# Kernel optimization log

Measured on AMD Instinct MI355X. Metric: run time of the kernel, lower is better.

The kernel has to match this reference:

```python
import jax, jax.numpy as jnp
from jax import lax
import numpy as np

# ---- constants (from Coords2Elec init kwargs) ----
BOX = 128          # box_size
RES = 1.0          # resolution (Angstrom / voxel)
EPS_IN = 6.5
EPS_OUT = 79.0
ION = 1.0          # ion_size
WAT = 1.4          # wat_size (water probe radius)
ASIGMA = 2.0
KAPPA02 = 0.8486   # debye_length kwarg, passed to solver as kappa0^2
QCONV = 7046.52    # charge_conv
D = 2              # gaussian sharpness divisor
W = 9              # scatter support window per axis (covers ~2.7 sigma)
N_ITER = 20        # Jacobi sweeps for the Poisson-Boltzmann solve

# staggered-grid offsets for the 4 eps channels: face-centered x/y/z + ion grid
OFFSETS = ((0.5, 0.0, 0.0), (0.0, 0.5, 0.0), (0.0, 0.0, 0.5), (0.5, 0.5, 0.5))


def _scatter_gauss(coords, sigma, mask, offset):
    """Scatter per-atom Gaussian density onto a staggered [B,BOX,BOX,BOX] grid.
    coords [B,N,3], sigma [B,N], mask [B,N], offset: 3 floats in voxel units."""
    B, N, _ = coords.shape
    off = jnp.asarray(offset, coords.dtype)
    offs = jnp.arange(W)
    # window base index so that grid node positions (idx+off)*RES bracket the atom
    base = jnp.floor(coords / RES - off).astype(jnp.int32) - W // 2     # [B,N,3]
    idx = base[..., None] + offs                                         # [B,N,3,W]
    gpos = (idx.astype(coords.dtype) + off[None, None, :, None]) * RES   # [B,N,3,W]
    d2 = (gpos - coords[..., None]) ** 2
    wax = jnp.exp(-d2 / (2.0 * sigma[:, :, None, None] ** 2))            # [B,N,3,W]
    w = (wax[:, :, 0, :, None, None] * wax[:, :, 1, None, :, None]
         * wax[:, :, 2, None, None, :]) * mask[:, :, None, None, None]   # [B,N,W,W,W]
    b_idx = jnp.broadcast_to(jnp.arange(B)[:, None, None, None, None], w.shape)
    ix = jnp.broadcast_to(idx[:, :, 0, :, None, None], w.shape)
    iy = jnp.broadcast_to(idx[:, :, 1, None, :, None], w.shape)
    iz = jnp.broadcast_to(idx[:, :, 2, None, None, :], w.shape)
    grid = jnp.zeros((B, BOX, BOX, BOX), coords.dtype)
    return grid.at[b_idx, ix, iy, iz].add(w, mode='drop')


def _scatter_q(coords, charge, mask):
    """Trilinear scatter of per-atom charges onto node grid [B,BOX,BOX,BOX]."""
    B, N, _ = coords.shape
    u = coords / RES
    i0 = jnp.floor(u).astype(jnp.int32)                 # [B,N,3]
    f = u - i0
    wpair = jnp.stack([1.0 - f, f], -1)                 # [B,N,3,2]
    ipair = jnp.stack([i0, i0 + 1], -1)                 # [B,N,3,2]
    w = (wpair[:, :, 0, :, None, None] * wpair[:, :, 1, None, :, None]
         * wpair[:, :, 2, None, None, :]) * (charge * mask)[:, :, None, None, None]
    b_idx = jnp.broadcast_to(jnp.arange(B)[:, None, None, None, None], w.shape)
    ix = jnp.broadcast_to(ipair[:, :, 0, :, None, None], w.shape)
    iy = jnp.broadcast_to(ipair[:, :, 1, None, :, None], w.shape)
    iz = jnp.broadcast_to(ipair[:, :, 2, None, None, :], w.shape)
    grid = jnp.zeros((B, BOX, BOX, BOX), coords.dtype)
    return grid.at[b_idx, ix, iy, iz].add(w, mode='drop')


def _face_nb(a, axis):
    """Face eps of the (i-1) cell along axis; boundary padded with EPS_OUT."""
    lead = jnp.full_like(lax.slice_in_dim(a, 0, 1, axis=axis), EPS_OUT)
    return jnp.concatenate([lead, lax.slice_in_dim(a, 0, a.shape[axis] - 1, axis=axis)], axis=axis)


def _phi_nb(phi, axis, d):
    """Neighbor potential phi[i+d] along spatial axis, zero (Dirichlet) outside."""
    z = jnp.zeros_like(lax.slice_in_dim(phi, 0, 1, axis=axis))
    if d > 0:
        return jnp.concatenate([lax.slice_in_dim(phi, 1, phi.shape[axis], axis=axis), z], axis=axis)
    return jnp.concatenate([z, lax.slice_in_dim(phi, 0, phi.shape[axis] - 1, axis=axis)], axis=axis)


def _qeps2phi(Q, Eps):
    """Fixed-iteration Jacobi solve of the linearized Poisson-Boltzmann stencil."""
    ex, ey, ez, ek = Eps[:, 0], Eps[:, 1], Eps[:, 2], Eps[:, 3]
    exm, eym, ezm = _face_nb(ex, 1), _face_nb(ey, 2), _face_nb(ez, 3)
    lam = jnp.clip((ek - EPS_IN) / (EPS_OUT - EPS_IN), 0.0, 1.0)  # ion accessibility
    denom = ex + exm + ey + eym + ez + ezm + KAPPA02 * RES * RES * lam
    src = 4.0 * jnp.pi * Q * RES

    def body(i, phi):
        num = (ex * _phi_nb(phi, 1, +1) + exm * _phi_nb(phi, 1, -1)
               + ey * _phi_nb(phi, 2, +1) + eym * _phi_nb(phi, 2, -1)
               + ez * _phi_nb(phi, 3, +1) + ezm * _phi_nb(phi, 3, -1) + src)
        return num / denom

    return lax.fori_loop(0, N_ITER, body, jnp.zeros_like(Q))


def setup_inputs() -> dict:
    key = jax.random.key(0)
    k1, k2, k3, k4 = jax.random.split(key, 4)
    B, N = 4, 4096
    coords = jax.random.uniform(k1, (B, N, 3), jnp.float32) * ((BOX - 1) * RES)
    charges = jax.random.normal(k2, (B, N), jnp.float32) * 0.5     # partial charges
    radii = 1.0 + jax.random.uniform(k3, (B, N), jnp.float32)      # 1..2 Angstrom
    assigned_params = jnp.stack([charges, radii], -1)              # [B,N,2]
    num_atoms = jax.random.randint(k4, (B,), N // 2, N + 1, jnp.int32)
    return {"coords": coords, "assigned_params": assigned_params, "num_atoms": num_atoms}


def reference(coords, assigned_params, num_atoms):
    B, N, _ = coords.shape
    mask = (jnp.arange(N)[None, :] < num_atoms[:, None]).astype(coords.dtype)
    charge = assigned_params[..., 0]
    radii = assigned_params[..., 1]
    sig_eps = (radii + WAT) / D   # solvent-excluded Gaussian width
    sig_ion = (radii + ION) / D   # ion-excluded Gaussian width
    rho = jnp.stack([
        _scatter_gauss(coords, sig_eps if c < 3 else sig_ion, mask, OFFSETS[c])
        for c in range(4)], axis=1)                     # [B,4,BOX,BOX,BOX]
    rho = jnp.clip(rho, 0.0, 1.0)
    eps = rho * (EPS_IN - EPS_OUT) + EPS_OUT
    q = _scatter_q(coords, charge, mask) * QCONV        # [B,BOX,BOX,BOX]
    phi = _qeps2phi(q, eps)
    return q, eps, phi
```

## Files before the change

kernel.cpp:

```cpp
#include <hip/hip_runtime.h>
#include <hip/hip_fp16.h>
#include <math.h>

static constexpr int   B_    = 4;
static constexpr int   N_    = 4096;
static constexpr int   BOX_  = 128;
static constexpr long long VOX_ = 1LL * BOX_ * BOX_ * BOX_;
static constexpr float EPS_IN_C  = 6.5f;
static constexpr float EPS_OUT_C = 79.0f;
static constexpr float QCONV_C   = 7046.52f;
static constexpr float KAPPA02_C = 0.8486f;
static constexpr float FOURPI_C  = 12.566370614359172f;

__global__ void scatter_q_kernel(const float* __restrict__ coords,
                                 const float* __restrict__ params,
                                 const int*   __restrict__ num_atoms,
                                 float* __restrict__ q)
{
    int a = blockIdx.x * blockDim.x + threadIdx.x;
    if (a >= B_ * N_) return;
    int b = a >> 12;
    int n = a & (N_ - 1);
    if (n >= num_atoms[b]) return;

    float cx = coords[3 * a + 0];
    float cy = coords[3 * a + 1];
    float cz = coords[3 * a + 2];
    float chg = params[2 * a + 0] * QCONV_C;

    int ix0 = (int)floorf(cx), iy0 = (int)floorf(cy), iz0 = (int)floorf(cz);
    float fx = cx - (float)ix0, fy = cy - (float)iy0, fz = cz - (float)iz0;
    float wx[2] = {1.0f - fx, fx};
    float wy[2] = {1.0f - fy, fy};
    float wz[2] = {1.0f - fz, fz};

    float* qb = q + (long long)b * VOX_;
#pragma unroll
    for (int dx = 0; dx < 2; ++dx) {
        int ix = ix0 + dx;
        if ((unsigned)ix >= 128u) continue;
#pragma unroll
        for (int dy = 0; dy < 2; ++dy) {
            int iy = iy0 + dy;
            if ((unsigned)iy >= 128u) continue;
#pragma unroll
            for (int dz = 0; dz < 2; ++dz) {
                int iz = iz0 + dz;
                if ((unsigned)iz >= 128u) continue;
                atomicAdd(&qb[((long long)ix * 128 + iy) * 128 + iz],
                          chg * wx[dx] * wy[dy] * wz[dz]);
            }
        }
    }
}

#define CAND_CAP 512
#define CHUNK 32

__global__ void eps_gather_v2(const float* __restrict__ coords,
                              const float* __restrict__ params,
                              const int*   __restrict__ num_atoms,
                              float* __restrict__ eps)
{
    int tileId = blockIdx.x;
    int b  = tileId >> 12;
    int t  = tileId & 4095;
    int tx = ((t >> 8) & 15) << 3;
    int ty = ((t >> 4) & 15) << 3;
    int tz = (t & 15) << 3;

    __shared__ float sx[CAND_CAP], sy[CAND_CAP], sz[CAND_CAP], sr[CAND_CAP];
    __shared__ float wts[CHUNK][9][8];
    __shared__ int s_cnt;
    if (threadIdx.x == 0) s_cnt = 0;
    __syncthreads();

    int na = num_atoms[b];
    const float* cb = coords + (size_t)b * N_ * 3;
    const float* pb = params + (size_t)b * N_ * 2;

    float lox = (float)tx - 4.0f, hix = (float)tx + 12.5f;
    float loy = (float)ty - 4.0f, hiy = (float)ty + 12.5f;
    float loz = (float)tz - 4.0f, hiz = (float)tz + 12.5f;
    bool wx_ = (tx == 120), wy_ = (ty == 120), wz_ = (tz == 120);
    for (int n = threadIdx.x; n < na; n += blockDim.x) {
        float cx = cb[3 * n], cy = cb[3 * n + 1], cz = cb[3 * n + 2];
        bool okx = (cx >= lox && cx < hix) || (wx_ && cx < 4.5f);
        bool oky = (cy >= loy && cy < hiy) || (wy_ && cy < 4.5f);
        bool okz = (cz >= loz && cz < hiz) || (wz_ && cz < 4.5f);
        if (okx && oky && okz) {
            int slot = atomicAdd(&s_cnt, 1);
            if (slot < CAND_CAP) {
                sx[slot] = cx; sy[slot] = cy; sz[slot] = cz;
                sr[slot] = pb[2 * n + 1];
            }
        }
    }
    __syncthreads();
    int cnt = min(s_cnt, CAND_CAP);

    int lz = threadIdx.x & 7;
    int ly = (threadIdx.x >> 3) & 7;
    int lx = threadIdx.x >> 6;

    float r0 = 0.0f, r1 = 0.0f, r2 = 0.0f, r3 = 0.0f;

    for (int k0 = 0; k0 < cnt; k0 += CHUNK) {
        int nC = min(CHUNK, cnt - k0);
        __syncthreads();
        for (int w = threadIdx.x; w < nC * 72; w += 512) {
            int ka  = w / 72;
            int rem = w - ka * 72;
            int vi  = rem >> 3;
            int pos = rem & 7;
            int axis = vi / 3, var = vi - axis * 3;
            int k = k0 + ka;
            float c     = (axis == 0) ? sx[k] : (axis == 1) ? sy[k] : sz[k];
            int   torig = (axis == 0) ? tx    : (axis == 1) ? ty    : tz;
            float r = sr[k];
            float sig = (var == 2) ? (r + 1.0f) * 0.5f : (r + 1.4f) * 0.5f;
            float off = (var == 0) ? 0.0f : 0.5f;
            float inv2s2 = 1.0f / (2.0f * sig * sig);
            int i = torig + pos;
            int base = (int)floorf(c - off) - 4;
            float wv = 0.0f;
            if ((unsigned)(i - base) <= 8u) {
                float d = (float)i + off - c;
                wv = expf(-d * d * inv2s2);
            } else if ((unsigned)(i - 128 - base) <= 8u) {
                float d = (float)(i - 128) + off - c;
                wv = expf(-d * d * inv2s2);
            }
            wts[ka][vi][pos] = wv;
        }
        __syncthreads();
        for (int ka = 0; ka < nC; ++ka) {
            float xE0 = wts[ka][0][lx], xE5 = wts[ka][1][lx], xI5 = wts[ka][2][lx];
            float yE0 = wts[ka][3][ly], yE5 = wts[ka][4][ly], yI5 = wts[ka][5][ly];
            float zE0 = wts[ka][6][lz], zE5 = wts[ka][7][lz], zI5 = wts[ka][8][lz];
            r0 += xE5 * yE0 * zE0;
            r1 += xE0 * yE5 * zE0;
            r2 += xE0 * yE0 * zE5;
            r3 += xI5 * yI5 * zI5;
        }
    }

    int ix = tx + lx, iy = ty + ly, iz = tz + lz;
    size_t sp = ((size_t)ix * 128 + iy) * 128 + iz;
    float* eb = eps + (size_t)b * 4 * VOX_;
    eb[sp]                    = EPS_OUT_C + (EPS_IN_C - EPS_OUT_C) * fminf(fmaxf(r0, 0.0f), 1.0f);
    eb[sp + (size_t)VOX_]     = EPS_OUT_C + (EPS_IN_C - EPS_OUT_C) * fminf(fmaxf(r1, 0.0f), 1.0f);
    eb[sp + (size_t)VOX_ * 2] = EPS_OUT_C + (EPS_IN_C - EPS_OUT_C) * fminf(fmaxf(r2, 0.0f), 1.0f);
    eb[sp + (size_t)VOX_ * 3] = EPS_OUT_C + (EPS_IN_C - EPS_OUT_C) * fminf(fmaxf(r3, 0.0f), 1.0f);
}

__global__ void coef_pack4(const float* __restrict__ eps,
                           const float* __restrict__ q,
                           uint4* __restrict__ coef,
                           float* __restrict__ phi1)
{
    int tid = blockIdx.x * blockDim.x + threadIdx.x;
    size_t g4 = (size_t)tid * 4;
    int b  = (int)(g4 >> 21);
    size_t sp = g4 & (size_t)(VOX_ - 1);
    int x  = (int)(sp >> 14);
    int y  = (int)((sp >> 7) & 127);
    int z4 = (int)(sp & 127);

    const float* E = eps + (size_t)b * 4 * (size_t)VOX_;
    float4 ex4 = *reinterpret_cast<const float4*>(E + sp);
    float4 ey4 = *reinterpret_cast<const float4*>(E + sp + (size_t)VOX_);
    float4 ez4 = *reinterpret_cast<const float4*>(E + sp + (size_t)VOX_ * 2);
    float4 ek4 = *reinterpret_cast<const float4*>(E + sp + (size_t)VOX_ * 3);
    float4 eo  = make_float4(EPS_OUT_C, EPS_OUT_C, EPS_OUT_C, EPS_OUT_C);
    float4 exm4 = (x > 0) ? *reinterpret_cast<const float4*>(E + sp - 16384) : eo;
    float4 eym4 = (y > 0) ? *reinterpret_cast<const float4*>(E + sp + (size_t)VOX_ - 128) : eo;
    float ezm0  = (z4 > 0) ? E[sp + (size_t)VOX_ * 2 - 1] : EPS_OUT_C;
    float4 q4  = *reinterpret_cast<const float4*>(q + g4);

    float exA[4]  = {ex4.x, ex4.y, ex4.z, ex4.w};
    float eyA[4]  = {ey4.x, ey4.y, ey4.z, ey4.w};
    float ezA[4]  = {ez4.x, ez4.y, ez4.z, ez4.w};
    float ekA[4]  = {ek4.x, ek4.y, ek4.z, ek4.w};
    float exmA[4] = {exm4.x, exm4.y, exm4.z, exm4.w};
    float eymA[4] = {eym4.x, eym4.y, eym4.z, eym4.w};
    float ezmA[4] = {ezm0, ez4.x, ez4.y, ez4.z};
    float qA[4]   = {q4.x, q4.y, q4.z, q4.w};

    float ph[4];
#pragma unroll
    for (int j = 0; j < 4; ++j) {
        float lam = (ekA[j] - EPS_IN_C) / (EPS_OUT_C - EPS_IN_C);
        lam = fminf(fmaxf(lam, 0.0f), 1.0f);
        float denom = exA[j] + exmA[j] + eyA[j] + eymA[j] + ezA[j] + ezmA[j]
                    + KAPPA02_C * lam;
        float rcp = 1.0f / denom;

        __half2 h01 = __floats2half2_rn(exA[j] * rcp, exmA[j] * rcp);
        __half2 h23 = __floats2half2_rn(eyA[j] * rcp, eymA[j] * rcp);
        __half2 h45 = __floats2half2_rn(ezA[j] * rcp, ezmA[j] * rcp);
        __half2 h67 = __floats2half2_rn(FOURPI_C * qA[j] * rcp, 0.0f);
        uint4 u;
        u.x = *(unsigned int*)&h01;
        u.y = *(unsigned int*)&h23;
        u.z = *(unsigned int*)&h45;
        u.w = *(unsigned int*)&h67;
        coef[g4 + j] = u;
        ph[j] = __half22float2(h67).x;
    }
    *reinterpret_cast<float4*>(phi1 + g4) = make_float4(ph[0], ph[1], ph[2], ph[3]);
}

#define TY 8
#define TZ 32
#define RY (TY + 2)
#define RZ (TZ + 2)
#define PYD (TY + 4)
#define PZD (TZ + 4)
#define SEG 16

__global__ __launch_bounds__(256)
void jacobi_f2p(const uint4* __restrict__ coef,
                const float* __restrict__ pin,
                float* __restrict__ pout)
{
    int bid = blockIdx.x;
    int xs = bid & 7;
    int zt = (bid >> 3) & 3;
    int yt = (bid >> 5) & 15;
    int b  = bid >> 9;
    int x_lo = xs * SEG, x_hi = x_lo + SEG - 1;
    int y0 = yt * TY, z0 = zt * TZ;

    __shared__ float P[3][PYD * PZD];
    __shared__ float S[3][RY * RZ];

    int tid = threadIdx.x;
    int oy = tid >> 5, oz = tid & 31;

    const uint4* cb = coef + (size_t)b * VOX_;
    const float* pb = pin  + (size_t)b * VOX_;
    float*       ob = pout + (size_t)b * VOX_;

    int e1_i  = (oy + 1) * RZ + (oz + 1);
    int g1y = y0 + oy, g1z = z0 + oz;
    int e1_off = g1y * 128 + g1z;
    int e1_p0 = (oy + 2) * PZD + (oz + 2);
    bool has2 = (tid < 84);
    int e2_ry = 0, e2_rz = 0;
    if (tid < 34)      { e2_ry = 0;      e2_rz = tid; }
    else if (tid < 68) { e2_ry = RY - 1; e2_rz = tid - 34; }
    else if (tid < 84) { int t2 = tid - 68; e2_ry = 1 + (t2 >> 1); e2_rz = (t2 & 1) * (RZ - 1); }
    int e2_i = e2_ry * RZ + e2_rz;
    int g2y = y0 - 1 + e2_ry, g2z = z0 - 1 + e2_rz;
    bool e2_ok = ((unsigned)g2y < 128u) && ((unsigned)g2z < 128u);
    int e2_off = min(max(g2y, 0), 127) * 128 + min(max(g2z, 0), 127);
    int e2_p0 = (e2_ry + 1) * PZD + (e2_rz + 1);
    int p1_py = tid / PZD, p1_pz = tid - p1_py * PZD;
    int p1y = y0 - 2 + p1_py, p1z = z0 - 2 + p1_pz;
    bool p1_ok = ((unsigned)p1y < 128u) && ((unsigned)p1z < 128u);
    int p1_off = min(max(p1y, 0), 127) * 128 + min(max(p1z, 0), 127);
    int p2i = tid + 256;
    bool hasP2 = (p2i < PYD * PZD);
    int p2_py = p2i / PZD, p2_pz = p2i - p2_py * PZD;
    int p2y = y0 - 2 + p2_py, p2z = z0 - 2 + p2_pz;
    bool p2_ok = hasP2 && ((unsigned)p2y < 128u) && ((unsigned)p2z < 128u);
    int p2_off = min(max(p2y, 0), 127) * 128 + min(max(p2z, 0), 127);

    const float* ps0 = pb + (size_t)min(max(x_lo - 2, 0), 127) * 16384;
    float pfA = ps0[p1_off];
    float pfB = hasP2 ? ps0[p2_off] : 0.0f;
    uint4 cf1 = make_uint4(0u, 0u, 0u, 0u);
    uint4 cf2 = make_uint4(0u, 0u, 0u, 0u);
    uint4 hold = make_uint4(0u, 0u, 0u, 0u);
    uint4 cnew = make_uint4(0u, 0u, 0u, 0u);

    for (int x = x_lo - 2; x <= x_hi + 2; ++x) {
        int s0 = (x + 3) % 3;
        int s1 = (x + 2) % 3;
        int s2 = (x + 1) % 3;
        bool xin = (x >= 0 && x < 128);

        P[s0][tid] = (xin && p1_ok) ? pfA : 0.0f;
        if (hasP2) P[s0][p2i] = (xin && p2_ok) ? pfB : 0.0f;
        asm volatile("s_waitcnt lgkmcnt(0)" ::: "memory");
        __builtin_amdgcn_s_barrier();

        if (x < x_hi + 2) {
            const float* ps = pb + (size_t)min(max(x + 1, 0), 127) * 16384;
            pfA = ps[p1_off];
            if (hasP2) pfB = ps[p2_off];
        }

        if (x >= x_lo) {
            int k = x - 1;
            bool kin = ((unsigned)k < 128u);
            {
                float v = 0.0f;
                if (kin) {
                    const __half2* h = reinterpret_cast<const __half2*>(&cf1);
                    float2 a01 = __half22float2(h[0]);
                    float2 a23 = __half22float2(h[1]);
                    float2 a45 = __half22float2(h[2]);
                    float2 a67 = __half22float2(h[3]);
                    v = a01.x * P[s0][e1_p0]
                      + a01.y * P[s2][e1_p0]
                      + a23.x * P[s1][e1_p0 + PZD]
                      + a23.y * P[s1][e1_p0 - PZD]
                      + a45.x * P[s1][e1_p0 + 1]
                      + a45.y * P[s1][e1_p0 - 1]
                      + a67.x;
                }
                S[s1][e1_i] = v;
                cnew = cf1;
            }
            if (has2) {
                float v = 0.0f;
                if (kin && e2_ok) {
                    const __half2* h = reinterpret_cast<const __half2*>(&cf2);
                    float2 a01 = __half22float2(h[0]);
                    float2 a23 = __half22float2(h[1]);
                    float2 a45 = __half22float2(h[2]);
                    float2 a67 = __half22float2(h[3]);
                    v = a01.x * P[s0][e2_p0]
                      + a01.y * P[s2][e2_p0]
                      + a23.x * P[s1][e2_p0 + PZD]
                      + a23.y * P[s1][e2_p0 - PZD]
                      + a45.x * P[s1][e2_p0 + 1]
                      + a45.y * P[s1][e2_p0 - 1]
                      + a67.x;
                }
                S[s1][e2_i] = v;
            }
        }
        if (x >= x_lo - 1 && x <= x_hi + 1) {
            const uint4* cs = cb + (size_t)min(max(x, 0), 127) * 16384;
            cf1 = cs[e1_off];
            if (has2) cf2 = cs[e2_off];
        }
        asm volatile("s_waitcnt lgkmcnt(0)" ::: "memory");
        __builtin_amdgcn_s_barrier();

        int xo = x - 2;
        if (xo >= x_lo) {
            const __half2* h = reinterpret_cast<const __half2*>(&hold);
            float2 a01 = __half22float2(h[0]);
            float2 a23 = __half22float2(h[1]);
            float2 a45 = __half22float2(h[2]);
            float2 a67 = __half22float2(h[3]);
            int j0 = e1_i;
            float out = a01.x * S[s1][j0]
                      + a01.y * S[s0][j0]
                      + a23.x * S[s2][j0 + RZ]
                      + a23.y * S[s2][j0 - RZ]
                      + a45.x * S[s2][j0 + 1]
                      + a45.y * S[s2][j0 - 1]
                      + a67.x;
            ob[(size_t)xo * 16384 + e1_off] = out;
        }
        hold = cnew;
    }
}

__global__ void jacobi_v3(const uint4* __restrict__ coef,
                          const float* __restrict__ pin,
                          float* __restrict__ pout)
{
    int tid = blockIdx.x * blockDim.x + threadIdx.x;
    size_t g4 = (size_t)tid * 4;
    int z4 = (int)(g4 & 127);
    int y  = (int)((g4 >> 7) & 127);
    int x  = (int)((g4 >> 14) & 127);

    float4 pcv = *reinterpret_cast<const float4*>(pin + g4);
    float4 z4v = make_float4(0.f, 0.f, 0.f, 0.f);
    float4 pxpv = (x < 127) ? *reinterpret_cast<const float4*>(pin + g4 + 16384) : z4v;
    float4 pxmv = (x > 0)   ? *reinterpret_cast<const float4*>(pin + g4 - 16384) : z4v;
    float4 pypv = (y < 127) ? *reinterpret_cast<const float4*>(pin + g4 + 128)   : z4v;
    float4 pymv = (y > 0)   ? *reinterpret_cast<const float4*>(pin + g4 - 128)   : z4v;
    float zpE = (z4 < 124) ? pin[g4 + 4] : 0.0f;
    float zmE = (z4 > 0)   ? pin[g4 - 1] : 0.0f;

    float pxp[4] = {pxpv.x, pxpv.y, pxpv.z, pxpv.w};
    float pxm[4] = {pxmv.x, pxmv.y, pxmv.z, pxmv.w};
    float pyp[4] = {pypv.x, pypv.y, pypv.z, pypv.w};
    float pym[4] = {pymv.x, pymv.y, pymv.z, pymv.w};
    float pzp[4] = {pcv.y, pcv.z, pcv.w, zpE};
    float pzm[4] = {zmE, pcv.x, pcv.y, pcv.z};

    float out[4];
#pragma unroll
    for (int j = 0; j < 4; ++j) {
        uint4 cu = coef[g4 + j];
        const __half2* h = reinterpret_cast<const __half2*>(&cu);
        float2 a01 = __half22float2(h[0]);
        float2 a23 = __half22float2(h[1]);
        float2 a45 = __half22float2(h[2]);
        float2 a67 = __half22float2(h[3]);
        out[j] = a01.x * pxp[j] + a01.y * pxm[j]
               + a23.x * pyp[j] + a23.y * pym[j]
               + a45.x * pzp[j] + a45.y * pzm[j]
               + a67.x;
    }
    *reinterpret_cast<float4*>(pout + g4) = make_float4(out[0], out[1], out[2], out[3]);
}

__global__ void jacobi_v2(const float* __restrict__ eps,
                          const float* __restrict__ q,
                          const float* __restrict__ pin,
                          float* __restrict__ pout)
{
    int bxy = blockIdx.x;
    int b = bxy >> 14;
    int x = (bxy >> 7) & 127;
    int y = bxy & 127;
    int z = threadIdx.x;

    size_t sp = ((size_t)x * 128 + y) * 128 + z;
    size_t g  = (size_t)b * (size_t)VOX_ + sp;
    const float* E = eps + (size_t)b * 4 * (size_t)VOX_;

    float ex = E[sp];
    float ey = E[sp + (size_t)VOX_];
    float ez = E[sp + (size_t)VOX_ * 2];
    float ek = E[sp + (size_t)VOX_ * 3];
    float exm = (x > 0) ? E[sp - 16384]                 : EPS_OUT_C;
    float eym = (y > 0) ? E[sp + (size_t)VOX_ - 128]    : EPS_OUT_C;
    float ezm = (z > 0) ? E[sp + (size_t)VOX_ * 2 - 1]  : EPS_OUT_C;

    float lam = (ek - EPS_IN_C) / (EPS_OUT_C - EPS_IN_C);
    lam = fminf(fmaxf(lam, 0.0f), 1.0f);
    float denom = ex + exm + ey + eym + ez + ezm + KAPPA02_C * lam;

    float pxp = (x < 127) ? pin[g + 16384] : 0.0f;
    float pxm = (x > 0)   ? pin[g - 16384] : 0.0f;
    float pyp = (y < 127) ? pin[g + 128]   : 0.0f;
    float pym = (y > 0)   ? pin[g - 128]   : 0.0f;
    float pzp = (z < 127) ? pin[g + 1]     : 0.0f;
    float pzm = (z > 0)   ? pin[g - 1]     : 0.0f;

    float num = ex * pxp + exm * pxm + ey * pyp + eym * pym
              + ez * pzp + ezm * pzm + FOURPI_C * q[g];
    pout[g] = num / denom;
}

extern "C" void kernel_launch(void* const* d_in, const int* in_sizes, int n_in,
                              void* d_out, int out_size, void* d_ws, size_t ws_size,
                              hipStream_t stream)
{
    const float* coords    = (const float*)d_in[0];
    const float* params    = (const float*)d_in[1];
    const int*   num_atoms = (const int*)d_in[2];

    float* q   = (float*)d_out;
    float* eps = q + (size_t)B_ * VOX_;
    float* phi = eps + (size_t)B_ * 4 * VOX_;

    hipMemsetAsync(q, 0, (size_t)B_ * VOX_ * sizeof(float), stream);

    scatter_q_kernel<<<(B_ * N_ + 255) / 256, 256, 0, stream>>>(coords, params, num_atoms, q);
    eps_gather_v2<<<B_ * 4096, 512, 0, stream>>>(coords, params, num_atoms, eps);

    size_t coefBytes = (size_t)B_ * VOX_ * sizeof(uint4);
    size_t need = coefBytes + (size_t)B_ * VOX_ * sizeof(float);

    if (ws_size >= need) {
        uint4* coefA = (uint4*)d_ws;
        float* tmp   = (float*)((char*)d_ws + coefBytes);
        coef_pack4<<<(int)(B_ * VOX_ / 4 / 256), 256, 0, stream>>>(eps, q, coefA, phi);
        const float* cur = phi;
        for (int it = 1; it <= 9; ++it) {
            float* dst = (it & 1) ? tmp : phi;
            jacobi_f2p<<<B_ * 16 * 4 * 8, 256, 0, stream>>>(coefA, cur, dst);
            cur = dst;
        }
        jacobi_v3<<<(int)(B_ * VOX_ / 4 / 256), 256, 0, stream>>>(coefA, cur, phi);
    } else {
        hipMemsetAsync(phi, 0, (size_t)B_ * VOX_ * sizeof(float), stream);
        float* tmp = (float*)d_ws;
        int jb = B_ * 128 * 128;
        const float* cur = phi;
        for (int it = 1; it <= 20; ++it) {
            float* dst = (it & 1) ? tmp : phi;
            jacobi_v2<<<jb, 128, 0, stream>>>(eps, q, cur, dst);
            cur = dst;
        }
    }
}
```

Baseline: 721.0 us.

## Share one atom candidate scan across a column of z tiles in eps gather

The eps gather kernel now gives each block a whole column of 8x8 x-y tiles and loops over the 16 z tiles inside the block. Each block reads the full atom list from global memory once, keeps the atoms that pass the x/y window test, and then refilters that shared list by z for each tile. Before, every one of the 4096 tiles per batch rescanned every atom, and this change is meant to remove that repeated scan. In exchange the grid shrinks 16x, the z tiles run one after another with extra barriers, and the 512-entry candidate cap now has to hold every atom in the column rather than in one tile.

```diff
diff --git a/kernel.cpp b/kernel.cpp
--- a/kernel.cpp
+++ b/kernel.cpp
@@ -57,21 +57,22 @@
 #define CAND_CAP 512
 #define CHUNK 32
 
-__global__ void eps_gather_v2(const float* __restrict__ coords,
-                              const float* __restrict__ params,
-                              const int*   __restrict__ num_atoms,
-                              float* __restrict__ eps)
-{
-    int tileId = blockIdx.x;
-    int b  = tileId >> 12;
-    int t  = tileId & 4095;
-    int tx = ((t >> 8) & 15) << 3;
-    int ty = ((t >> 4) & 15) << 3;
-    int tz = (t & 15) << 3;
+__global__ __launch_bounds__(512)
+void eps_gather_v3(const float* __restrict__ coords,
+                   const float* __restrict__ params,
+                   const int*   __restrict__ num_atoms,
+                   float* __restrict__ eps)
+{
+    int bid = blockIdx.x;
+    int b   = bid >> 8;
+    int txi = (bid >> 4) & 15;
+    int tyi = bid & 15;
+    int tx = txi << 3, ty = tyi << 3;
 
     __shared__ float sx[CAND_CAP], sy[CAND_CAP], sz[CAND_CAP], sr[CAND_CAP];
     __shared__ float wts[CHUNK][9][8];
-    __shared__ int s_cnt;
+    __shared__ int  fidx[CAND_CAP];
+    __shared__ int  s_cnt, s_fcnt;
     if (threadIdx.x == 0) s_cnt = 0;
     __syncthreads();
 
@@ -81,14 +82,12 @@
 
     float lox = (float)tx - 4.0f, hix = (float)tx + 12.5f;
     float loy = (float)ty - 4.0f, hiy = (float)ty + 12.5f;
-    float loz = (float)tz - 4.0f, hiz = (float)tz + 12.5f;
-    bool wx_ = (tx == 120), wy_ = (ty == 120), wz_ = (tz == 120);
-    for (int n = threadIdx.x; n < na; n += blockDim.x) {
+    bool wx_ = (tx == 120), wy_ = (ty == 120);
+    for (int n = threadIdx.x; n < na; n += 512) {
         float cx = cb[3 * n], cy = cb[3 * n + 1], cz = cb[3 * n + 2];
         bool okx = (cx >= lox && cx < hix) || (wx_ && cx < 4.5f);
         bool oky = (cy >= loy && cy < hiy) || (wy_ && cy < 4.5f);
-        bool okz = (cz >= loz && cz < hiz) || (wz_ && cz < 4.5f);
-        if (okx && oky && okz) {
+        if (okx && oky) {
             int slot = atomicAdd(&s_cnt, 1);
             if (slot < CAND_CAP) {
                 sx[slot] = cx; sy[slot] = cy; sz[slot] = cz;
@@ -103,55 +102,77 @@
     int ly = (threadIdx.x >> 3) & 7;
     int lx = threadIdx.x >> 6;
 
-    float r0 = 0.0f, r1 = 0.0f, r2 = 0.0f, r3 = 0.0f;
-
-    for (int k0 = 0; k0 < cnt; k0 += CHUNK) {
-        int nC = min(CHUNK, cnt - k0);
+    float* eb = eps + (size_t)b * 4 * VOX_;
+
+    for (int tzi = 0; tzi < 16; ++tzi) {
+        int tz = tzi << 3;
+
         __syncthreads();
-        for (int w = threadIdx.x; w < nC * 72; w += 512) {
-            int ka  = w / 72;
-            int rem = w - ka * 72;
-            int vi  = rem >> 3;
-            int pos = rem & 7;
-            int axis = vi / 3, var = vi - axis * 3;
-            int k = k0 + ka;
-            float c     = (axis == 0) ? sx[k] : (axis == 1) ? sy[k] : sz[k];
-            int   torig = (axis == 0) ? tx    : (axis == 1) ? ty    : tz;
-            float r = sr[k];
-            float sig = (var == 2) ? (r + 1.0f) * 0.5f : (r + 1.4f) * 0.5f;
-            float off = (var == 0) ? 0.0f : 0.5f;
-            float inv2s2 = 1.0f / (2.0f * sig * sig);
-            int i = torig + pos;
-            int base = (int)floorf(c - off) - 4;
-            float wv = 0.0f;
-            if ((unsigned)(i - base) <= 8u) {
-                float d = (float)i + off - c;
-                wv = expf(-d * d * inv2s2);
-            } else if ((unsigned)(i - 128 - base) <= 8u) {
-                float d = (float)(i - 128) + off - c;
-                wv = expf(-d * d * inv2s2);
-            }
-            wts[ka][vi][pos] = wv;
-        }
+        if (threadIdx.x == 0) s_fcnt = 0;
         __syncthreads();
-        for (int ka = 0; ka < nC; ++ka) {
-            float xE0 = wts[ka][0][lx], xE5 = wts[ka][1][lx], xI5 = wts[ka][2][lx];
-            float yE0 = wts[ka][3][ly], yE5 = wts[ka][4][ly], yI5 = wts[ka][5][ly];
-            float zE0 = wts[ka][6][lz], zE5 = wts[ka][7][lz], zI5 = wts[ka][8][lz];
-            r0 += xE5 * yE0 * zE0;
-            r1 += xE0 * yE5 * zE0;
-            r2 += xE0 * yE0 * zE5;
-            r3 += xI5 * yI5 * zI5;
-        }
-    }
-
-    int ix = tx + lx, iy = ty + ly, iz = tz + lz;
-    size_t sp = ((size_t)ix * 128 + iy) * 128 + iz;
-    float* eb = eps + (size_t)b * 4 * VOX_;
-    eb[sp]                    = EPS_OUT_C + (EPS_IN_C - EPS_OUT_C) * fminf(fmaxf(r0, 0.0f), 1.0f);
-    eb[sp + (size_t)VOX_]     = EPS_OUT_C + (EPS_IN_C - EPS_OUT_C) * fminf(fmaxf(r1, 0.0f), 1.0f);
-    eb[sp + (size_t)VOX_ * 2] = EPS_OUT_C + (EPS_IN_C - EPS_OUT_C) * fminf(fmaxf(r2, 0.0f), 1.0f);
-    eb[sp + (size_t)VOX_ * 3] = EPS_OUT_C + (EPS_IN_C - EPS_OUT_C) * fminf(fmaxf(r3, 0.0f), 1.0f);
+        {
+            float loz = (float)tz - 4.0f, hiz = (float)tz + 12.5f;
+            bool wz_ = (tz == 120);
+            for (int i = threadIdx.x; i < cnt; i += 512) {
+                float cz = sz[i];
+                if ((cz >= loz && cz < hiz) || (wz_ && cz < 4.5f)) {
+                    int s = atomicAdd(&s_fcnt, 1);
+                    fidx[s] = i;
+                }
+            }
+        }
+        __syncthreads();
+        int fcnt = s_fcnt;
+
+        float r0 = 0.0f, r1 = 0.0f, r2 = 0.0f, r3 = 0.0f;
+
+        for (int k0 = 0; k0 < fcnt; k0 += CHUNK) {
+            int nC = min(CHUNK, fcnt - k0);
+            __syncthreads();
+            for (int w = threadIdx.x; w < nC * 72; w += 512) {
+                int ka  = w / 72;
+                int rem = w - ka * 72;
+                int vi  = rem >> 3;
+                int pos = rem & 7;
+                int axis = vi / 3, var = vi - axis * 3;
+                int k = fidx[k0 + ka];
+                float c     = (axis == 0) ? sx[k] : (axis == 1) ? sy[k] : sz[k];
+                int   torig = (axis == 0) ? tx    : (axis == 1) ? ty    : tz;
+                float r = sr[k];
+                float sig = (var == 2) ? (r + 1.0f) * 0.5f : (r + 1.4f) * 0.5f;
+                float off = (var == 0) ? 0.0f : 0.5f;
+                float inv2s2 = 1.0f / (2.0f * sig * sig);
+                int i = torig + pos;
+                int base = (int)floorf(c - off) - 4;
+                float wv = 0.0f;
+                if ((unsigned)(i - base) <= 8u) {
+                    float d = (float)i + off - c;
+                    wv = expf(-d * d * inv2s2);
+                } else if ((unsigned)(i - 128 - base) <= 8u) {
+                    float d = (float)(i - 128) + off - c;
+                    wv = expf(-d * d * inv2s2);
+                }
+                wts[ka][vi][pos] = wv;
+            }
+            __syncthreads();
+            for (int ka = 0; ka < nC; ++ka) {
+                float xE0 = wts[ka][0][lx], xE5 = wts[ka][1][lx], xI5 = wts[ka][2][lx];
+                float yE0 = wts[ka][3][ly], yE5 = wts[ka][4][ly], yI5 = wts[ka][5][ly];
+                float zE0 = wts[ka][6][lz], zE5 = wts[ka][7][lz], zI5 = wts[ka][8][lz];
+                r0 += xE5 * yE0 * zE0;
+                r1 += xE0 * yE5 * zE0;
+                r2 += xE0 * yE0 * zE5;
+                r3 += xI5 * yI5 * zI5;
+            }
+        }
+
+        int ix = tx + lx, iy = ty + ly, iz = tz + lz;
+        size_t sp = ((size_t)ix * 128 + iy) * 128 + iz;
+        eb[sp]                    = EPS_OUT_C + (EPS_IN_C - EPS_OUT_C) * fminf(fmaxf(r0, 0.0f), 1.0f);
+        eb[sp + (size_t)VOX_]     = EPS_OUT_C + (EPS_IN_C - EPS_OUT_C) * fminf(fmaxf(r1, 0.0f), 1.0f);
+        eb[sp + (size_t)VOX_ * 2] = EPS_OUT_C + (EPS_IN_C - EPS_OUT_C) * fminf(fmaxf(r2, 0.0f), 1.0f);
+        eb[sp + (size_t)VOX_ * 3] = EPS_OUT_C + (EPS_IN_C - EPS_OUT_C) * fminf(fmaxf(r3, 0.0f), 1.0f);
+    }
 }
 
 __global__ void coef_pack4(const float* __restrict__ eps,
@@ -459,7 +480,7 @@
     hipMemsetAsync(q, 0, (size_t)B_ * VOX_ * sizeof(float), stream);
 
     scatter_q_kernel<<<(B_ * N_ + 255) / 256, 256, 0, stream>>>(coords, params, num_atoms, q);
-    eps_gather_v2<<<B_ * 4096, 512, 0, stream>>>(coords, params, num_atoms, eps);
+    eps_gather_v3<<<B_ * 16 * 16, 512, 0, stream>>>(coords, params, num_atoms, eps);
 
     size_t coefBytes = (size_t)B_ * VOX_ * sizeof(uint4);
     size_t need = coefBytes + (size_t)B_ * VOX_ * sizeof(float);
```

Result: no change. 719.4 us (-0.2%).
